# Performance work log

Measured on AMD Instinct MI355X. Metric: run time of the kernel, lower is better.

Reference implementation:

```python
import jax, jax.numpy as jnp
import numpy as np

EPS = 1e-8  # torch CosineSimilarity default eps
SIZE = 16
HIDDEN = 768


def setup_inputs() -> dict:
    key = jax.random.key(0)
    k1, k2, k3, k4, k5 = jax.random.split(key, 5)
    x = jax.random.normal(k1, (4, 3, 224, 224), dtype=jnp.float32)
    # Conv2d(channel, hidden, kernel=1) -> weight (hidden, channel)
    pixel_w = jax.random.normal(k2, (HIDDEN, 3), dtype=jnp.float32) * 0.1
    pixel_b = jax.random.normal(k3, (HIDDEN,), dtype=jnp.float32) * 0.1
    # Conv2d(channel, hidden, kernel=size, stride=size) -> weight (hidden, channel, size, size)
    patch_w = jax.random.normal(k4, (HIDDEN, 3, SIZE, SIZE), dtype=jnp.float32) * 0.02
    patch_b = jax.random.normal(k5, (HIDDEN,), dtype=jnp.float32) * 0.1
    return {"x": x, "pixel_w": pixel_w, "pixel_b": pixel_b,
            "patch_w": patch_w, "patch_b": patch_b}


def reference(x, pixel_w, pixel_b, patch_w, patch_b):
    B, C, H, W = x.shape
    D = pixel_w.shape[0]
    S = SIZE
    Hp, Wp = H // S, W // S
    Np = Hp * Wp  # number of patches (196)

    # pixel embeddings: 1x1 conv -> (B, H*W, D), row-major over (H, W)
    pixel = jnp.einsum('bchw,dc->bhwd', x, pixel_w) + pixel_b
    pixel = pixel.reshape(B, H * W, D)

    # patch embeddings: non-overlapping size x size conv (stride == kernel)
    xp = x.reshape(B, C, Hp, S, Wp, S)
    patch = jnp.einsum('bchpwq,dcpq->bhwd', xp, patch_w) + patch_b
    patch = patch.reshape(B, Np, D)

    # cosine similarity: normalize once, then a single tiled matmul
    pn = pixel / jnp.maximum(jnp.linalg.norm(pixel, axis=-1, keepdims=True), EPS)
    qn = patch / jnp.maximum(jnp.linalg.norm(patch, axis=-1, keepdims=True), EPS)
    SIM = jnp.einsum('bnd,bmd->bnm', pn, qn)  # (B, H*W, Np)
    SIM = SIM.reshape(B, S * S, Np, Np)

    # masked exp-sum over off-diagonal entries, then single log
    off_diag = ~jnp.eye(Np, dtype=bool)  # (Np, Np)
    s = jnp.where(off_diag, jnp.exp(SIM / 0.5), 0.0).sum()
    # -log(1/s) == log(s); .mean() on a scalar is a no-op
    return jnp.log(s)
```

## Files before the change

### kernel.cpp

```cpp
#include <hip/hip_runtime.h>
#include <math.h>

#define EPS 1e-8f
#define NPATCH 196
#define HW 50176
#define LOG2E 1.4426950408889634f

#define P5T_OFF 64
#define DJT_OFF 40960
#define PART_OFF 196608

typedef __attribute__((ext_vector_type(8))) short short8;
typedef __attribute__((ext_vector_type(4))) float f32x4;

static __device__ __forceinline__ unsigned short f2bf(float f) {
    unsigned u = __float_as_uint(f);
    u += 0x8000u + ((u >> 16) & 1u);
    return (unsigned short)(u >> 16);
}

static __device__ __forceinline__ short8 cvt8(float4 a, float4 b) {
    short8 o;
    o[0] = f2bf(a.x); o[1] = f2bf(a.y); o[2] = f2bf(a.z); o[3] = f2bf(a.w);
    o[4] = f2bf(b.x); o[5] = f2bf(b.y); o[6] = f2bf(b.z); o[7] = f2bf(b.w);
    return o;
}

__global__ __launch_bounds__(256) void k_gemm(const float* __restrict__ x,
                                              const float* __restrict__ pixw,
                                              const float* __restrict__ pixb,
                                              const float* __restrict__ paw,
                                              const float* __restrict__ pab,
                                              float* __restrict__ ws) {
    int t = threadIdx.x;
    int lane = t & 63, wv = t >> 6;
    int bid = blockIdx.x;
    int msup = bid / 49;
    int ntile = bid - msup * 49;
    int mtile = msup * 4 + wv;
    int m0 = mtile * 16, n0 = ntile * 16;
    int ra = lane & 15, kg = lane >> 4;

    const float* pa = paw + (size_t)(m0 + ra) * 768 + kg * 8;

    int gp = n0 + ra;
    int b = gp / NPATCH, m = gp - b * NPATCH;
    int hp = m / 14, wq = m - hp * 14;
    const float* xb0 = x + (size_t)b * (3 * HW) + (hp * 16) * 224 + wq * 16;

    f32x4 acc = {0.f, 0.f, 0.f, 0.f};
    #pragma unroll 4
    for (int kk = 0; kk < 24; ++kk) {
        int k = kg * 8 + kk * 32;
        float4 a0 = *(const float4*)(pa + kk * 32);
        float4 a1 = *(const float4*)(pa + kk * 32 + 4);
        int c = k >> 8, rem = k & 255, pr = rem >> 4, q0 = rem & 15;
        const float* bs = xb0 + c * HW + pr * 224 + q0;
        float4 b0 = *(const float4*)bs;
        float4 b1 = *(const float4*)(bs + 4);
        acc = __builtin_amdgcn_mfma_f32_16x16x32_bf16(cvt8(a0, a1), cvt8(b0, b1),
                                                      acc, 0, 0, 0);
    }

    float sq = 0.f, d0 = 0.f, d1 = 0.f, d2 = 0.f, d3 = 0.f;
    #pragma unroll
    for (int i = 0; i < 4; ++i) {
        int d = m0 + kg * 4 + i;
        float v = acc[i] + pab[d];
        sq = fmaf(v, v, sq);
        d0 = fmaf(pixw[d*3+0], v, d0);
        d1 = fmaf(pixw[d*3+1], v, d1);
        d2 = fmaf(pixw[d*3+2], v, d2);
        d3 = fmaf(pixb[d],     v, d3);
    }
    sq += __shfl_down(sq, 32); d0 += __shfl_down(d0, 32);
    d1 += __shfl_down(d1, 32); d2 += __shfl_down(d2, 32);
    d3 += __shfl_down(d3, 32);
    sq += __shfl_down(sq, 16); d0 += __shfl_down(d0, 16);
    d1 += __shfl_down(d1, 16); d2 += __shfl_down(d2, 16);
    d3 += __shfl_down(d3, 16);
    if (lane < 16) {
        int g = n0 + lane;
        ws[P5T_OFF + (size_t)g * 48 + mtile] = sq;
        *(float4*)&ws[DJT_OFF + ((size_t)g * 48 + mtile) * 4] =
            make_float4(d0, d1, d2, d3);
    }
}

__global__ __launch_bounds__(512) void k_pixel(const float* __restrict__ x,
                                               const float* __restrict__ pixw,
                                               const float* __restrict__ pixb,
                                               float* __restrict__ ws) {
    __shared__ float gtmp[8][10];
    __shared__ float gram_s[10];
    __shared__ float raw[NPATCH][5];
    __shared__ float gq[NPATCH][4];
    __shared__ float red[8];
    int t = threadIdx.x;
    int bid = blockIdx.x;
    int b = bid / 98;

    {
        float g[10];
        #pragma unroll
        for (int j = 0; j < 10; ++j) g[j] = 0.f;
        for (int d = t; d < 768; d += 512) {
            float w0 = pixw[d*3+0], w1 = pixw[d*3+1], w2 = pixw[d*3+2], bb = pixb[d];
            g[0] = fmaf(w0, w0, g[0]); g[1] = fmaf(w0, w1, g[1]);
            g[2] = fmaf(w0, w2, g[2]); g[3] = fmaf(w0, bb, g[3]);
            g[4] = fmaf(w1, w1, g[4]); g[5] = fmaf(w1, w2, g[5]);
            g[6] = fmaf(w1, bb, g[6]); g[7] = fmaf(w2, w2, g[7]);
            g[8] = fmaf(w2, bb, g[8]); g[9] = fmaf(bb, bb, g[9]);
        }
        #pragma unroll
        for (int off = 32; off; off >>= 1)
            #pragma unroll
            for (int j = 0; j < 10; ++j) g[j] += __shfl_down(g[j], off);
        int wvv = t >> 6, ln = t & 63;
        if (ln == 0)
            #pragma unroll
            for (int j = 0; j < 10; ++j) gtmp[wvv][j] = g[j];
    }

    if (t < 392) {
        int p = t >> 1, h = t & 1;
        int g = b * NPATCH + p;
        const float*  p5 = ws + P5T_OFF + (size_t)g * 48 + h * 24;
        const float4* dj = (const float4*)(ws + DJT_OFF) + (size_t)g * 48 + h * 24;
        float n2 = 0.f, e0 = 0.f, e1 = 0.f, e2 = 0.f, e3 = 0.f;
        #pragma unroll 8
        for (int i = 0; i < 24; ++i) {
            n2 += p5[i];
            float4 v = dj[i];
            e0 += v.x; e1 += v.y; e2 += v.z; e3 += v.w;
        }
        n2 += __shfl_down(n2, 1); e0 += __shfl_down(e0, 1);
        e1 += __shfl_down(e1, 1); e2 += __shfl_down(e2, 1);
        e3 += __shfl_down(e3, 1);
        if (h == 0) {
            raw[p][0] = n2; raw[p][1] = e0; raw[p][2] = e1;
            raw[p][3] = e2; raw[p][4] = e3;
        }
    }
    __syncthreads();
    if (t < 10)
        gram_s[t] = gtmp[0][t] + gtmp[1][t] + gtmp[2][t] + gtmp[3][t] +
                    gtmp[4][t] + gtmp[5][t] + gtmp[6][t] + gtmp[7][t];
    if (t < NPATCH) {
        float rq = 1.0f / fmaxf(sqrtf(raw[t][0]), EPS);
        gq[t][0] = raw[t][1] * rq;
        gq[t][1] = raw[t][2] * rq;
        gq[t][2] = raw[t][3] * rq;
        gq[t][3] = raw[t][4] * rq;
    }
    __syncthreads();

    int hw = (bid - b * 98) * 512 + t;
    const float* xb = x + (size_t)b * (3 * HW);
    float c0 = xb[hw], c1 = xb[hw + HW], c2 = xb[hw + 2 * HW];

    float G0 = gram_s[0], G1 = gram_s[1], G2 = gram_s[2], G3 = gram_s[3];
    float G4 = gram_s[4], G5 = gram_s[5], G6 = gram_s[6], G7 = gram_s[7];
    float G8 = gram_s[8], G9 = gram_s[9];
    float n2 = G9;
    n2 = fmaf(G0, c0 * c0, n2);
    n2 = fmaf(G4, c1 * c1, n2);
    n2 = fmaf(G7, c2 * c2, n2);
    float cross = fmaf(G1, c0 * c1, fmaf(G2, c0 * c2, fmaf(G5, c1 * c2,
                  fmaf(G3, c0, fmaf(G6, c1, G8 * c2)))));
    n2 = fmaf(2.0f, cross, n2);

    float rnp = 1.0f / fmaxf(sqrtf(n2), EPS);
    float es = 2.0f * rnp * LOG2E;
    float a0 = c0 * es, a1 = c1 * es, a2 = c2 * es;

    float sum = 0.0f;
    #pragma unroll 4
    for (int m = 0; m < NPATCH; ++m) {
        float4 g = *(const float4*)gq[m];
        float tt = fmaf(a0, g.x, fmaf(a1, g.y, fmaf(a2, g.z, es * g.w)));
        sum += __builtin_amdgcn_exp2f(tt);
    }
    {
        int ne = hw % NPATCH;
        float4 g = *(const float4*)gq[ne];
        float tt = fmaf(a0, g.x, fmaf(a1, g.y, fmaf(a2, g.z, es * g.w)));
        sum -= __builtin_amdgcn_exp2f(tt);
    }
    #pragma unroll
    for (int off = 32; off; off >>= 1) sum += __shfl_down(sum, off);
    int wvv = t >> 6, ln = t & 63;
    if (ln == 0) red[wvv] = sum;
    __syncthreads();
    if (t == 0) {
        float s = 0.f;
        #pragma unroll
        for (int w = 0; w < 8; ++w) s += red[w];
        ws[PART_OFF + bid] = s;
    }
}

__global__ __launch_bounds__(512) void k_log(const float* __restrict__ ws,
                                             float* __restrict__ out) {
    __shared__ float red[8];
    int t = threadIdx.x;
    float sum = (t < 392) ? ws[PART_OFF + t] : 0.f;
    #pragma unroll
    for (int off = 32; off; off >>= 1) sum += __shfl_down(sum, off);
    int wv = t >> 6, ln = t & 63;
    if (ln == 0) red[wv] = sum;
    __syncthreads();
    if (t == 0) {
        float s = 0.f;
        #pragma unroll
        for (int w = 0; w < 8; ++w) s += red[w];
        out[0] = logf(s);
    }
}

extern "C" void kernel_launch(void* const* d_in, const int* in_sizes, int n_in,
                              void* d_out, int out_size, void* d_ws, size_t ws_size,
                              hipStream_t stream) {
    (void)in_sizes; (void)n_in; (void)out_size; (void)ws_size;
    const float* x    = (const float*)d_in[0];
    const float* pixw = (const float*)d_in[1];
    const float* pixb = (const float*)d_in[2];
    const float* paw  = (const float*)d_in[3];
    const float* pab  = (const float*)d_in[4];
    float* ws  = (float*)d_ws;
    float* out = (float*)d_out;

    hipLaunchKernelGGL(k_gemm,  dim3(588), dim3(256), 0, stream,
                       x, pixw, pixb, paw, pab, ws);
    hipLaunchKernelGGL(k_pixel, dim3(392), dim3(512), 0, stream,
                       x, pixw, pixb, ws);
    hipLaunchKernelGGL(k_log,   dim3(1),   dim3(512), 0, stream, ws, out);
}
```

Measured before the change: 54.10 us.

## Pre-convert GEMM operands to bf16 in a prep kernel; fuse final log via atomic counter

Adds a prep kernel that converts the patch weights and the im2col'd image patches to bf16 once into workspace. The GEMM inner loop then does plain short8 loads with no per-iteration conversion or address math. The separate log kernel is removed: the last k_pixel block, found through an atomic counter, does the final reduction. This trades one launch for another and adds extra workspace traffic in exchange for a simpler GEMM loop.

```diff
diff --git a/kernel.cpp b/kernel.cpp
--- a/kernel.cpp
+++ b/kernel.cpp
@@ -6,9 +6,12 @@
 #define HW 50176
 #define LOG2E 1.4426950408889634f
 
+#define COUNT_OFF 0
 #define P5T_OFF 64
 #define DJT_OFF 40960
 #define PART_OFF 196608
+#define WA_OFF 212992
+#define XPB_OFF 360448
 
 typedef __attribute__((ext_vector_type(8))) short short8;
 typedef __attribute__((ext_vector_type(4))) float f32x4;
@@ -19,19 +22,44 @@
     return (unsigned short)(u >> 16);
 }
 
-static __device__ __forceinline__ short8 cvt8(float4 a, float4 b) {
-    short8 o;
-    o[0] = f2bf(a.x); o[1] = f2bf(a.y); o[2] = f2bf(a.z); o[3] = f2bf(a.w);
-    o[4] = f2bf(b.x); o[5] = f2bf(b.y); o[6] = f2bf(b.z); o[7] = f2bf(b.w);
-    return o;
-}
-
-__global__ __launch_bounds__(256) void k_gemm(const float* __restrict__ x,
-                                              const float* __restrict__ pixw,
+__global__ __launch_bounds__(256) void k_prep(const float* __restrict__ x,
+                                              const float* __restrict__ paw,
+                                              float* __restrict__ ws) {
+    int t = threadIdx.x;
+    int bid = blockIdx.x;
+    if (bid == 0 && t == 0) *(int*)(ws + COUNT_OFF) = 0;
+    if (bid < 288) {
+        int f8 = bid * 256 + t;
+        const float4* src = (const float4*)paw + (size_t)f8 * 2;
+        float4 a = src[0], b = src[1];
+        short8 o;
+        o[0] = f2bf(a.x); o[1] = f2bf(a.y); o[2] = f2bf(a.z); o[3] = f2bf(a.w);
+        o[4] = f2bf(b.x); o[5] = f2bf(b.y); o[6] = f2bf(b.z); o[7] = f2bf(b.w);
+        *(short8*)((unsigned short*)(ws + WA_OFF) + (size_t)f8 * 8) = o;
+    } else {
+        int f8 = (bid - 288) * 256 + t;
+        int gp = f8 / 96;
+        int e = (f8 - gp * 96) * 8;
+        int b = gp / NPATCH, m = gp - b * NPATCH;
+        int hp = m / 14, wq = m - hp * 14;
+        int c = e >> 8, rem = e & 255, pr = rem >> 4, q0 = rem & 15;
+        const float* src = x + ((size_t)(b * 3 + c) * 224 + hp * 16 + pr) * 224
+                             + wq * 16 + q0;
+        float4 a = *(const float4*)src;
+        float4 b2 = *(const float4*)(src + 4);
+        short8 o;
+        o[0] = f2bf(a.x);  o[1] = f2bf(a.y);  o[2] = f2bf(a.z);  o[3] = f2bf(a.w);
+        o[4] = f2bf(b2.x); o[5] = f2bf(b2.y); o[6] = f2bf(b2.z); o[7] = f2bf(b2.w);
+        *(short8*)((unsigned short*)(ws + XPB_OFF) + (size_t)gp * 768 + e) = o;
+    }
+}
+
+__global__ __launch_bounds__(256) void k_gemm(const float* __restrict__ pixw,
                                               const float* __restrict__ pixb,
-                                              const float* __restrict__ paw,
                                               const float* __restrict__ pab,
                                               float* __restrict__ ws) {
+    const unsigned short* WA  = (const unsigned short*)(ws + WA_OFF);
+    const unsigned short* XPB = (const unsigned short*)(ws + XPB_OFF);
     int t = threadIdx.x;
     int lane = t & 63, wv = t >> 6;
     int bid = blockIdx.x;
@@ -40,28 +68,15 @@
     int mtile = msup * 4 + wv;
     int m0 = mtile * 16, n0 = ntile * 16;
     int ra = lane & 15, kg = lane >> 4;
-
-    const float* pa = paw + (size_t)(m0 + ra) * 768 + kg * 8;
-
-    int gp = n0 + ra;
-    int b = gp / NPATCH, m = gp - b * NPATCH;
-    int hp = m / 14, wq = m - hp * 14;
-    const float* xb0 = x + (size_t)b * (3 * HW) + (hp * 16) * 224 + wq * 16;
-
+    const short8* pa = (const short8*)(WA  + (size_t)(m0 + ra) * 768 + kg * 8);
+    const short8* pb = (const short8*)(XPB + (size_t)(n0 + ra) * 768 + kg * 8);
     f32x4 acc = {0.f, 0.f, 0.f, 0.f};
-    #pragma unroll 4
+    #pragma unroll 6
     for (int kk = 0; kk < 24; ++kk) {
-        int k = kg * 8 + kk * 32;
-        float4 a0 = *(const float4*)(pa + kk * 32);
-        float4 a1 = *(const float4*)(pa + kk * 32 + 4);
-        int c = k >> 8, rem = k & 255, pr = rem >> 4, q0 = rem & 15;
-        const float* bs = xb0 + c * HW + pr * 224 + q0;
-        float4 b0 = *(const float4*)bs;
-        float4 b1 = *(const float4*)(bs + 4);
-        acc = __builtin_amdgcn_mfma_f32_16x16x32_bf16(cvt8(a0, a1), cvt8(b0, b1),
-                                                      acc, 0, 0, 0);
-    }
-
+        short8 a = pa[kk * 4];
+        short8 b = pb[kk * 4];
+        acc = __builtin_amdgcn_mfma_f32_16x16x32_bf16(a, b, acc, 0, 0, 0);
+    }
     float sq = 0.f, d0 = 0.f, d1 = 0.f, d2 = 0.f, d3 = 0.f;
     #pragma unroll
     for (int i = 0; i < 4; ++i) {
@@ -90,12 +105,14 @@
 __global__ __launch_bounds__(512) void k_pixel(const float* __restrict__ x,
                                                const float* __restrict__ pixw,
                                                const float* __restrict__ pixb,
-                                               float* __restrict__ ws) {
+                                               float* __restrict__ ws,
+                                               float* __restrict__ out) {
     __shared__ float gtmp[8][10];
     __shared__ float gram_s[10];
     __shared__ float raw[NPATCH][5];
     __shared__ float gq[NPATCH][4];
     __shared__ float red[8];
+    __shared__ int is_last;
     int t = threadIdx.x;
     int bid = blockIdx.x;
     int b = bid / 98;
@@ -196,25 +213,31 @@
         float s = 0.f;
         #pragma unroll
         for (int w = 0; w < 8; ++w) s += red[w];
-        ws[PART_OFF + bid] = s;
-    }
-}
-
-__global__ __launch_bounds__(512) void k_log(const float* __restrict__ ws,
-                                             float* __restrict__ out) {
-    __shared__ float red[8];
-    int t = threadIdx.x;
-    float sum = (t < 392) ? ws[PART_OFF + t] : 0.f;
-    #pragma unroll
-    for (int off = 32; off; off >>= 1) sum += __shfl_down(sum, off);
-    int wv = t >> 6, ln = t & 63;
-    if (ln == 0) red[wv] = sum;
-    __syncthreads();
-    if (t == 0) {
-        float s = 0.f;
-        #pragma unroll
-        for (int w = 0; w < 8; ++w) s += red[w];
-        out[0] = logf(s);
+        __hip_atomic_store(&ws[PART_OFF + bid], s, __ATOMIC_RELEASE,
+                           __HIP_MEMORY_SCOPE_AGENT);
+        int old = __hip_atomic_fetch_add((int*)(ws + COUNT_OFF), 1,
+                                         __ATOMIC_ACQ_REL,
+                                         __HIP_MEMORY_SCOPE_AGENT);
+        is_last = (old == 391);
+    }
+    __syncthreads();
+
+    if (is_last) {
+        float v = 0.f;
+        if (t < 392)
+            v = __hip_atomic_load(&ws[PART_OFF + t], __ATOMIC_ACQUIRE,
+                                  __HIP_MEMORY_SCOPE_AGENT);
+        #pragma unroll
+        for (int off = 32; off; off >>= 1) v += __shfl_down(v, off);
+        __syncthreads();
+        if ((t & 63) == 0) red[t >> 6] = v;
+        __syncthreads();
+        if (t == 0) {
+            float s = 0.f;
+            #pragma unroll
+            for (int w = 0; w < 8; ++w) s += red[w];
+            out[0] = logf(s);
+        }
     }
 }
 
@@ -230,9 +253,9 @@
     float* ws  = (float*)d_ws;
     float* out = (float*)d_out;
 
+    hipLaunchKernelGGL(k_prep,  dim3(582), dim3(256), 0, stream, x, paw, ws);
     hipLaunchKernelGGL(k_gemm,  dim3(588), dim3(256), 0, stream,
-                       x, pixw, pixb, paw, pab, ws);
+                       pixw, pixb, pab, ws);
     hipLaunchKernelGGL(k_pixel, dim3(392), dim3(512), 0, stream,
-                       x, pixw, pixb, ws);
-    hipLaunchKernelGGL(k_log,   dim3(1),   dim3(512), 0, stream, ws, out);
-}
+                       x, pixw, pixb, ws, out);
+}
```

Measured after the change: 52.52 us. 2.9% less time.
